# Kernel tuning notes

Measured on AMD Instinct MI355X. Metric: run time of the kernel, lower is better.

## Reference

```python
import jax, jax.numpy as jnp
import numpy as np

B, N = 1, 512
CS, CZ, H, CH, PQ, PV = 384, 128, 12, 16, 4, 8
INF, EPS = 1e5, 1e-8
SOFTPLUS_INV_1 = 0.541324854612918


def _init_linear(key, fan_in, fan_out):
    kw, kb = jax.random.split(key)
    std = float(1.0 / np.sqrt(fan_in))
    w = jax.random.normal(kw, (fan_in, fan_out), dtype=jnp.float32) * std
    b = jnp.zeros((fan_out,), dtype=jnp.float32)
    return w, b


def setup_inputs() -> dict:
    key = jax.random.key(0)
    ks = jax.random.split(key, 12)
    s = jax.random.normal(ks[0], (B, N, CS), dtype=jnp.float32)
    z = jax.random.normal(ks[1], (B, N, N, CZ), dtype=jnp.float32) * 0.1
    # proper rotation matrices via QR of random Gaussians
    rot, _ = jnp.linalg.qr(jax.random.normal(ks[2], (B, N, 3, 3), dtype=jnp.float32))
    trans = jax.random.normal(ks[3], (B, N, 3), dtype=jnp.float32) * 10.0
    mask = jnp.ones((B, N), dtype=jnp.float32)
    w_q, b_q = _init_linear(ks[4], CS, H * CH)
    w_kv, b_kv = _init_linear(ks[5], CS, 2 * H * CH)
    w_qp, b_qp = _init_linear(ks[6], CS, H * PQ * 3)
    w_kvp, b_kvp = _init_linear(ks[7], CS, H * (PQ + PV) * 3)
    w_b, b_b = _init_linear(ks[8], CZ, H)
    head_weights = jnp.full((H,), SOFTPLUS_INV_1, dtype=jnp.float32)
    concat_dim = H * (CZ + CH + PV * 4)
    # 'final' init -> zeros
    w_out = jnp.zeros((concat_dim, CS), dtype=jnp.float32)
    b_out = jnp.zeros((CS,), dtype=jnp.float32)
    return dict(s=s, z=z, rot=rot, trans=trans, mask=mask,
                w_q=w_q, b_q=b_q, w_kv=w_kv, b_kv=b_kv,
                w_qp=w_qp, b_qp=b_qp, w_kvp=w_kvp, b_kvp=b_kvp,
                w_b=w_b, b_b=b_b, head_weights=head_weights,
                w_out=w_out, b_out=b_out)


def reference(s, z, rot, trans, mask,
              w_q, b_q, w_kv, b_kv, w_qp, b_qp, w_kvp, b_kvp,
              w_b, b_b, head_weights, w_out, b_out):
    # scalar q/k/v: [B,N,H,CH]
    q = (s @ w_q + b_q).reshape(B, N, H, CH)
    kv = (s @ w_kv + b_kv).reshape(B, N, H, 2 * CH)
    k, v = kv[..., :CH], kv[..., CH:]

    def make_points(w, b, P):
        p = s @ w + b                                   # [B,N,3*H*P] (x|y|z chunks)
        p = jnp.moveaxis(p.reshape(B, N, 3, H * P), -2, -1)  # [B,N,H*P,3]
        p = jnp.einsum('bnij,bnpj->bnpi', rot, p) + trans[:, :, None]  # global frame
        return p.reshape(B, N, H, P, 3)

    q_pts = make_points(w_qp, b_qp, PQ)                 # [B,N,H,PQ,3]
    kv_pts = make_points(w_kvp, b_kvp, PQ + PV)
    k_pts, v_pts = kv_pts[..., :PQ, :], kv_pts[..., PQ:, :]

    # scalar QK attention + pair bias
    a = jnp.einsum('bqhc,bkhc->bhqk', q, k) * float(np.sqrt(1.0 / (3 * CH)))
    b_bias = z @ w_b + b_b                              # [B,N,N,H]
    a = a + float(np.sqrt(1.0 / 3.0)) * jnp.moveaxis(b_bias, -1, -3)

    # squared point-distance attention
    d = q_pts[:, :, None] - k_pts[:, None]              # [B,N,N,H,PQ,3]
    pt_att = jnp.sum(d * d, axis=-1)                    # [B,N,N,H,PQ]
    hw = jax.nn.softplus(head_weights) * float(np.sqrt(1.0 / (3 * (PQ * 9.0 / 2))))
    pt_att = -0.5 * jnp.sum(pt_att * hw[None, None, None, :, None], axis=-1)  # [B,N,N,H]
    a = a + jnp.moveaxis(pt_att, -1, -3)                # [B,H,N,N]

    sq_mask = (mask[:, :, None] * mask[:, None, :] - 1.0) * INF
    a = jax.nn.softmax(a + sq_mask[:, None], axis=-1)   # [B,H,N,N]

    # standard value path
    o = jnp.einsum('bhqk,bkhc->bqhc', a, v).reshape(B, N, H * CH)
    # point value path, rotated back to local frame
    o_pt = jnp.einsum('bhqk,bkhpc->bqhpc', a, v_pts)    # [B,N,H,PV,3]
    o_pt = jnp.einsum('bnji,bnhpj->bnhpi', rot, o_pt - trans[:, :, None, None])
    o_pt_norm = jnp.sqrt(jnp.sum(o_pt ** 2, axis=-1) + EPS).reshape(B, N, H * PV)
    o_pt = o_pt.reshape(B, N, H * PV, 3)
    # pair-weighted path
    o_pair = jnp.einsum('bhqk,bqkc->bqhc', a, z).reshape(B, N, H * CZ)

    o_cat = jnp.concatenate(
        [o, o_pt[..., 0], o_pt[..., 1], o_pt[..., 2], o_pt_norm, o_pair], axis=-1)
    return o_cat @ w_out + b_out
```

## Files before the change

kernel.cpp:

```cpp
#include <hip/hip_runtime.h>
#include <math.h>

#define NRES 512
#define CSD  384
#define CZD  128

#define OFF_Q     0
#define OFF_KT    98304
#define OFF_VC    196608
#define OFF_QP    458752
#define OFF_KPT   532480
#define OFF_A     606208
#define OFF_OCAT  3751936
#define OFF_WCAT  4833280
#define OFF_BCAT  (OFF_WCAT + 442368)
#define OFF_PRAWQ OFF_A
#define OFF_PRAWK (OFF_A + 73728)
#define OFF_PART  OFF_A

__global__ __launch_bounds__(256) void k_wcat(
    const float* __restrict__ w_q, const float* __restrict__ b_q,
    const float* __restrict__ w_kv, const float* __restrict__ b_kv,
    const float* __restrict__ w_qp, const float* __restrict__ b_qp,
    const float* __restrict__ w_kvp, const float* __restrict__ b_kvp,
    float* __restrict__ wcat, float* __restrict__ bcat)
{
    const int idx = blockIdx.x * 256 + threadIdx.x;
    if (idx < 442368) {
        const int k = idx / 1152, c = idx % 1152;
        float v;
        if (c < 192)      v = w_q[k*192 + c];
        else if (c < 576) v = w_kv[k*384 + (c - 192)];
        else if (c < 720) v = w_qp[k*144 + (c - 576)];
        else              v = w_kvp[k*432 + (c - 720)];
        wcat[idx] = v;
    } else if (idx < 443520) {
        const int c = idx - 442368;
        float v;
        if (c < 192)      v = b_q[c];
        else if (c < 576) v = b_kv[c - 192];
        else if (c < 720) v = b_qp[c - 576];
        else              v = b_kvp[c - 720];
        bcat[c] = v;
    }
}

__global__ __launch_bounds__(256) void k_proj2(
    const float* __restrict__ s, const float* __restrict__ wcat, const float* __restrict__ bcat,
    float* __restrict__ q, float* __restrict__ kkT, float* __restrict__ vcomb,
    float* __restrict__ praw_q, float* __restrict__ praw_kv)
{
    const int ct = blockIdx.x;
    const int n0 = blockIdx.y * 32;
    const int t = threadIdx.x;

    __shared__ float sT[32][34];
    __shared__ float wt[32][36];

    const int lr = t >> 3, lc4 = t & 7;
    const int tr = t >> 4, tc = t & 15;
    float4 sv4, wv4;

    sv4 = *(const float4*)&s[(n0 + lr) * CSD + lc4 * 4];
    wv4 = *(const float4*)&wcat[lr * 1152 + ct * 32 + lc4 * 4];
    sT[lc4*4+0][lr] = sv4.x; sT[lc4*4+1][lr] = sv4.y; sT[lc4*4+2][lr] = sv4.z; sT[lc4*4+3][lr] = sv4.w;
    *(float4*)&wt[lr][lc4*4] = wv4;
    __syncthreads();

    float a00 = 0.f, a01 = 0.f, a10 = 0.f, a11 = 0.f;

    for (int it = 0; it < 12; ++it) {
        if (it < 11) {
            const int k0 = (it + 1) * 32;
            sv4 = *(const float4*)&s[(n0 + lr) * CSD + k0 + lc4 * 4];
            wv4 = *(const float4*)&wcat[(k0 + lr) * 1152 + ct * 32 + lc4 * 4];
        }
        #pragma unroll
        for (int kx = 0; kx < 32; ++kx) {
            float2 ss = *(const float2*)&sT[kx][tr * 2];
            float2 ww = *(const float2*)&wt[kx][tc * 2];
            a00 += ss.x * ww.x; a01 += ss.x * ww.y;
            a10 += ss.y * ww.x; a11 += ss.y * ww.y;
        }
        __syncthreads();
        if (it < 11) {
            sT[lc4*4+0][lr] = sv4.x; sT[lc4*4+1][lr] = sv4.y; sT[lc4*4+2][lr] = sv4.z; sT[lc4*4+3][lr] = sv4.w;
            *(float4*)&wt[lr][lc4*4] = wv4;
            __syncthreads();
        }
    }

    float accv[2][2] = {{a00, a01}, {a10, a11}};
    #pragma unroll
    for (int i = 0; i < 2; ++i) {
        const int n = n0 + tr * 2 + i;
        #pragma unroll
        for (int j = 0; j < 2; ++j) {
            const int gcol = ct * 32 + tc * 2 + j;
            const float v = accv[i][j] + bcat[gcol];
            if (gcol < 192) {
                q[n*192 + gcol] = v;
            } else if (gcol < 576) {
                int g = gcol - 192, h = g >> 5, cc = g & 31;
                if (cc < 16) kkT[(h*16 + cc)*NRES + n] = v;
                else         vcomb[n*NRES + h*16 + (cc-16)] = v;
            } else if (gcol < 720) {
                praw_q[n*144 + (gcol - 576)] = v;
            } else {
                praw_kv[n*432 + (gcol - 720)] = v;
            }
        }
    }
}

__global__ __launch_bounds__(256) void k_rot(
    const float* __restrict__ praw_q, const float* __restrict__ praw_kv,
    const float* __restrict__ rot, const float* __restrict__ trans,
    float* __restrict__ q_pts, float* __restrict__ kptsT, float* __restrict__ vcomb)
{
    const int idx = blockIdx.x * 256 + threadIdx.x;
    const int n = idx / 192, u = idx % 192;
    const float* R = rot + n*9;
    const float* T = trans + n*3;
    float px, py, pz;
    if (u < 48) {
        px = praw_q[n*144 + u]; py = praw_q[n*144 + 48 + u]; pz = praw_q[n*144 + 96 + u];
    } else {
        int pt = u - 48;
        px = praw_kv[n*432 + pt]; py = praw_kv[n*432 + 144 + pt]; pz = praw_kv[n*432 + 288 + pt];
    }
    float x  = R[0]*px + R[1]*py + R[2]*pz + T[0];
    float y  = R[3]*px + R[4]*py + R[5]*pz + T[1];
    float zc = R[6]*px + R[7]*py + R[8]*pz + T[2];
    if (u < 48) {
        int o = (n*48 + u)*3;
        q_pts[o] = x; q_pts[o+1] = y; q_pts[o+2] = zc;
    } else {
        int pt = u - 48;
        int h = pt / 12, pp = pt % 12;
        if (pp < 4) {
            int dim = (h*4 + pp)*3;
            kptsT[(dim+0)*NRES + n] = x;
            kptsT[(dim+1)*NRES + n] = y;
            kptsT[(dim+2)*NRES + n] = zc;
        } else {
            int u2 = (h*8 + (pp-4))*3;
            vcomb[n*NRES + 192 + u2+0] = x;
            vcomb[n*NRES + 192 + u2+1] = y;
            vcomb[n*NRES + 192 + u2+2] = zc;
        }
    }
}

__global__ __launch_bounds__(256) void k_row(
    const float* __restrict__ z,
    const float* __restrict__ q, const float* __restrict__ kkT, const float* __restrict__ vcomb,
    const float* __restrict__ q_pts, const float* __restrict__ kptsT,
    const float* __restrict__ w_b, const float* __restrict__ b_b,
    const float* __restrict__ head_weights, const float* __restrict__ mask,
    const float* __restrict__ rot, const float* __restrict__ trans,
    float* __restrict__ o_cat)
{
    const int qn = blockIdx.x;
    const int t = threadIdx.x;

    __shared__ float zt[64*129];
    __shared__ float wb[128*12];
    __shared__ float part[4][64][13];
    __shared__ float a_lds[12][520];
    __shared__ float q_lds[192];
    __shared__ float qp_lds[144];
    __shared__ float hw_lds[12];
    __shared__ float optraw[288];

    for (int i = t; i < 1536; i += 256) wb[i] = w_b[i];
    if (t < 192) q_lds[t] = q[qn*192 + t];
    if (t < 144) qp_lds[t] = q_pts[qn*144 + t];
    if (t < 12)  hw_lds[t] = logf(1.f + expf(head_weights[t])) * 0.13608276f;

    const int kx = t & 63, qr = t >> 6;
    for (int kt = 0; kt < 8; ++kt) {
        const int k0 = kt*64;
        __syncthreads();
        const float4* zp4 = (const float4*)(z + ((size_t)qn*NRES + k0)*CZD);
        #pragma unroll
        for (int r = 0; r < 8; ++r) {
            int idx = t + r*256;
            int kk2 = idx >> 5, c4 = idx & 31;
            float4 v4 = zp4[idx];
            float* dst = &zt[kk2*129 + c4*4];
            dst[0]=v4.x; dst[1]=v4.y; dst[2]=v4.z; dst[3]=v4.w;
        }
        __syncthreads();
        float acc[12];
        #pragma unroll
        for (int h = 0; h < 12; ++h) acc[h] = 0.f;
        const float* zrow = &zt[kx*129 + qr*32];
        const float* wbp = &wb[qr*32*12];
        for (int c = 0; c < 32; ++c) {
            float zv = zrow[c];
            #pragma unroll
            for (int h = 0; h < 12; ++h) acc[h] += zv * wbp[c*12+h];
        }
        #pragma unroll
        for (int h = 0; h < 12; ++h) part[qr][kx][h] = acc[h];
        __syncthreads();
        for (int d = t; d < 768; d += 256) {
            int h = d >> 6, k2 = d & 63;
            a_lds[h][k0+k2] = b_b[h] + part[0][k2][h] + part[1][k2][h]
                            + part[2][k2][h] + part[3][k2][h];
        }
    }
    __syncthreads();

    const float mq = mask[qn];
    for (int h = 0; h < 12; ++h) {
        float qv[16], qpv[12];
        #pragma unroll
        for (int c = 0; c < 16; ++c) qv[c] = q_lds[h*16+c];
        #pragma unroll
        for (int d = 0; d < 12; ++d) qpv[d] = qp_lds[h*12+d];
        const float hw = hw_lds[h];
        const float* kT  = kkT + h*16*NRES;
        const float* kpT = kptsT + h*12*NRES;
        #pragma unroll
        for (int r = 0; r < 2; ++r) {
            const int kn = t + r*256;
            float acc = 0.f;
            #pragma unroll
            for (int c = 0; c < 16; ++c) acc += qv[c] * kT[c*NRES + kn];
            acc *= 0.14433757f;
            acc += 0.57735027f * a_lds[h][kn];
            float dsum = 0.f;
            #pragma unroll
            for (int d = 0; d < 12; ++d) { float df = qpv[d] - kpT[d*NRES + kn]; dsum += df*df; }
            a_lds[h][kn] = acc - 0.5f*hw*dsum + (mq*mask[kn]-1.f)*100000.f;
        }
    }
    __syncthreads();

    {
        const int w = t >> 6, lane = t & 63;
        for (int h = w; h < 12; h += 4) {
            float m = -1e30f;
            #pragma unroll
            for (int i = 0; i < 8; ++i) m = fmaxf(m, a_lds[h][lane + i*64]);
            #pragma unroll
            for (int off = 32; off > 0; off >>= 1) m = fmaxf(m, __shfl_xor(m, off));
            float ss = 0.f;
            #pragma unroll
            for (int i = 0; i < 8; ++i) {
                float e = __expf(a_lds[h][lane + i*64] - m);
                a_lds[h][lane + i*64] = e;
                ss += e;
            }
            #pragma unroll
            for (int off = 32; off > 0; off >>= 1) ss += __shfl_xor(ss, off);
            float inv = 1.f / ss;
            #pragma unroll
            for (int i = 0; i < 8; ++i) a_lds[h][lane + i*64] *= inv;
        }
    }
    __syncthreads();

    {
        const int c4 = t & 31, kgrp = t >> 5;
        const float4* zp = (const float4*)(z + (size_t)qn*NRES*CZD) + c4;
        float4 acc4[12];
        #pragma unroll
        for (int h = 0; h < 12; ++h) acc4[h] = make_float4(0.f,0.f,0.f,0.f);

        #pragma unroll 4
        for (int kn = kgrp; kn < NRES; kn += 8) {
            float4 zv = zp[kn*32];
            #pragma unroll
            for (int h = 0; h < 12; ++h) {
                float av = a_lds[h][kn];
                acc4[h].x += av*zv.x; acc4[h].y += av*zv.y;
                acc4[h].z += av*zv.z; acc4[h].w += av*zv.w;
            }
        }
        #pragma unroll
        for (int h = 0; h < 12; ++h) {
            acc4[h].x += __shfl_xor(acc4[h].x, 32);
            acc4[h].y += __shfl_xor(acc4[h].y, 32);
            acc4[h].z += __shfl_xor(acc4[h].z, 32);
            acc4[h].w += __shfl_xor(acc4[h].w, 32);
        }
        float (*ppart)[12][128] = (float (*)[12][128])zt;
        const int wave = t >> 6;
        if ((t & 63) < 32) {
            #pragma unroll
            for (int h = 0; h < 12; ++h) {
                ppart[wave][h][c4*4+0] = acc4[h].x;
                ppart[wave][h][c4*4+1] = acc4[h].y;
                ppart[wave][h][c4*4+2] = acc4[h].z;
                ppart[wave][h][c4*4+3] = acc4[h].w;
            }
        }
        __syncthreads();
        for (int i = t; i < 1536; i += 256) {
            int h = i >> 7, c = i & 127;
            float v = ppart[0][h][c] + ppart[1][h][c] + ppart[2][h][c] + ppart[3][h][c];
            o_cat[qn*2112 + 576 + h*128 + c] = v;
        }
    }

    {
        const int u0 = t;
        const int h0 = (u0 < 192) ? (u0 >> 4) : (u0 - 192) / 24;
        const int u1v = (t < 224) ? (t + 256) : 479;
        const int h1 = (u1v - 192) / 24;
        float acc0 = 0.f, acc1 = 0.f;
        const float* vp = vcomb;
        #pragma unroll 8
        for (int kn = 0; kn < NRES; ++kn) {
            const float* row = vp + (size_t)kn*NRES;
            acc0 += a_lds[h0][kn] * row[u0];
            acc1 += a_lds[h1][kn] * row[u1v];
        }
        if (u0 < 192) o_cat[qn*2112 + u0] = acc0;
        else          optraw[u0 - 192] = acc0;
        if (t < 224)  optraw[t + 64] = acc1;
    }
    __syncthreads();

    if (t < 96) {
        const float* R = rot + qn*9;
        const float* T = trans + qn*3;
        float ox = optraw[t*3]   - T[0];
        float oy = optraw[t*3+1] - T[1];
        float oz = optraw[t*3+2] - T[2];
        float x  = R[0]*ox + R[3]*oy + R[6]*oz;
        float y  = R[1]*ox + R[4]*oy + R[7]*oz;
        float zc = R[2]*ox + R[5]*oy + R[8]*oz;
        float* ob = o_cat + qn*2112;
        ob[192 + t] = x;
        ob[288 + t] = y;
        ob[384 + t] = zc;
        ob[480 + t] = sqrtf(x*x + y*y + zc*zc + 1e-8f);
    }
}

__global__ __launch_bounds__(256) void k_out2(
    const float* __restrict__ o_cat, const float* __restrict__ w_out, float* __restrict__ part)
{
    const int ct = blockIdx.x;
    const int n0 = blockIdx.y * 32;
    const int kc = blockIdx.z;
    const int t = threadIdx.x;

    __shared__ float oT[32][34];
    __shared__ float wt[32][36];

    const int lr = t >> 3, lc4 = t & 7;
    const int tr = t >> 4, tc = t & 15;
    const int kbase = kc * 352;
    float4 ov4, wv4;

    ov4 = *(const float4*)&o_cat[(n0 + lr) * 2112 + kbase + lc4 * 4];
    wv4 = *(const float4*)&w_out[(kbase + lr) * 384 + ct * 32 + lc4 * 4];
    oT[lc4*4+0][lr] = ov4.x; oT[lc4*4+1][lr] = ov4.y; oT[lc4*4+2][lr] = ov4.z; oT[lc4*4+3][lr] = ov4.w;
    *(float4*)&wt[lr][lc4*4] = wv4;
    __syncthreads();

    float a00 = 0.f, a01 = 0.f, a10 = 0.f, a11 = 0.f;

    for (int it = 0; it < 11; ++it) {
        if (it < 10) {
            const int k0 = kbase + (it + 1) * 32;
            ov4 = *(const float4*)&o_cat[(n0 + lr) * 2112 + k0 + lc4 * 4];
            wv4 = *(const float4*)&w_out[(k0 + lr) * 384 + ct * 32 + lc4 * 4];
        }
        #pragma unroll
        for (int kx = 0; kx < 32; ++kx) {
            float2 oo = *(const float2*)&oT[kx][tr * 2];
            float2 ww = *(const float2*)&wt[kx][tc * 2];
            a00 += oo.x * ww.x; a01 += oo.x * ww.y;
            a10 += oo.y * ww.x; a11 += oo.y * ww.y;
        }
        __syncthreads();
        if (it < 10) {
            oT[lc4*4+0][lr] = ov4.x; oT[lc4*4+1][lr] = ov4.y; oT[lc4*4+2][lr] = ov4.z; oT[lc4*4+3][lr] = ov4.w;
            *(float4*)&wt[lr][lc4*4] = wv4;
            __syncthreads();
        }
    }

    float* pp = part + (size_t)kc * 196608;
    pp[(n0 + tr*2 + 0)*384 + ct*32 + tc*2 + 0] = a00;
    pp[(n0 + tr*2 + 0)*384 + ct*32 + tc*2 + 1] = a01;
    pp[(n0 + tr*2 + 1)*384 + ct*32 + tc*2 + 0] = a10;
    pp[(n0 + tr*2 + 1)*384 + ct*32 + tc*2 + 1] = a11;
}

__global__ __launch_bounds__(256) void k_red(
    const float* __restrict__ part, const float* __restrict__ b_out, float* __restrict__ out)
{
    const int i = blockIdx.x*256 + threadIdx.x;
    float acc = b_out[i % 384];
    #pragma unroll
    for (int dc = 0; dc < 6; ++dc) acc += part[(size_t)dc*196608 + i];
    out[i] = acc;
}

extern "C" void kernel_launch(void* const* d_in, const int* in_sizes, int n_in,
                              void* d_out, int out_size, void* d_ws, size_t ws_size,
                              hipStream_t stream) {
    (void)in_sizes; (void)n_in; (void)out_size; (void)ws_size;
    const float* s      = (const float*)d_in[0];
    const float* z      = (const float*)d_in[1];
    const float* rot    = (const float*)d_in[2];
    const float* trans  = (const float*)d_in[3];
    const float* mask   = (const float*)d_in[4];
    const float* w_q    = (const float*)d_in[5];
    const float* b_q    = (const float*)d_in[6];
    const float* w_kv   = (const float*)d_in[7];
    const float* b_kv   = (const float*)d_in[8];
    const float* w_qp   = (const float*)d_in[9];
    const float* b_qp   = (const float*)d_in[10];
    const float* w_kvp  = (const float*)d_in[11];
    const float* b_kvp  = (const float*)d_in[12];
    const float* w_b    = (const float*)d_in[13];
    const float* b_b    = (const float*)d_in[14];
    const float* hwts   = (const float*)d_in[15];
    const float* w_out  = (const float*)d_in[16];
    const float* b_out  = (const float*)d_in[17];
    float* out = (float*)d_out;
    float* ws  = (float*)d_ws;

    float* q      = ws + OFF_Q;
    float* kkT    = ws + OFF_KT;
    float* vcomb  = ws + OFF_VC;
    float* qp     = ws + OFF_QP;
    float* kptsT  = ws + OFF_KPT;
    float* ocat   = ws + OFF_OCAT;
    float* wcat   = ws + OFF_WCAT;
    float* bcat   = ws + OFF_BCAT;
    float* part   = ws + OFF_PART;
    float* praw_q  = ws + OFF_PRAWQ;
    float* praw_kv = ws + OFF_PRAWK;

    k_wcat<<<dim3(1733), dim3(256), 0, stream>>>(w_q, b_q, w_kv, b_kv, w_qp, b_qp, w_kvp, b_kvp, wcat, bcat);
    k_proj2<<<dim3(36, 16), dim3(256), 0, stream>>>(s, wcat, bcat, q, kkT, vcomb, praw_q, praw_kv);
    k_rot<<<dim3(384), dim3(256), 0, stream>>>(praw_q, praw_kv, rot, trans, qp, kptsT, vcomb);
    k_row<<<dim3(NRES), dim3(256), 0, stream>>>(z, q, kkT, vcomb, qp, kptsT,
        w_b, b_b, hwts, mask, rot, trans, ocat);
    k_out2<<<dim3(12, 16, 6), dim3(256), 0, stream>>>(ocat, w_out, part);
    k_red<<<dim3(768), dim3(256), 0, stream>>>(part, b_out, out);
}
```

Before: 149.8 us.

## Fuse row attention into single-pass online softmax with register-prefetched z tiles

Rewrites the per-query row kernel to stream z in 64-key tiles once, computing pair bias, logits, an online softmax with running max and sum, and the z, scalar-value and point-value accumulations per tile. This removes the second full read of the z row from global memory and the full 12x512 logit buffer in shared memory. The next z tile is prefetched into registers while the current one is processed. In exchange it adds rescaling work and more barriers per tile, and raises register pressure from the 12 float4 accumulators plus 8 staging float4s.

```diff
diff --git a/kernel.cpp b/kernel.cpp
--- a/kernel.cpp
+++ b/kernel.cpp
@@ -152,7 +152,7 @@
     }
 }
 
-__global__ __launch_bounds__(256) void k_row(
+__global__ __launch_bounds__(256) void k_row2(
     const float* __restrict__ z,
     const float* __restrict__ q, const float* __restrict__ kkT, const float* __restrict__ vcomb,
     const float* __restrict__ q_pts, const float* __restrict__ kptsT,
@@ -164,10 +164,13 @@
     const int qn = blockIdx.x;
     const int t = threadIdx.x;
 
-    __shared__ float zt[64*129];
-    __shared__ float wb[128*12];
+    __shared__ float zt[64][132];
+    __shared__ float wb[1536];
     __shared__ float part[4][64][13];
-    __shared__ float a_lds[12][520];
+    __shared__ float bt[12][64];
+    __shared__ float pt[12][66];
+    __shared__ float fs[12];
+    __shared__ float ss[12];
     __shared__ float q_lds[192];
     __shared__ float qp_lds[144];
     __shared__ float hw_lds[12];
@@ -177,151 +180,188 @@
     if (t < 192) q_lds[t] = q[qn*192 + t];
     if (t < 144) qp_lds[t] = q_pts[qn*144 + t];
     if (t < 12)  hw_lds[t] = logf(1.f + expf(head_weights[t])) * 0.13608276f;
-
-    const int kx = t & 63, qr = t >> 6;
+    const float mq = mask[qn];
+
+    const int kx = t & 63, hgrp = t >> 6;
+    const int c4 = t & 31, kgrp = t >> 5;
+
+    float m_run0 = -1e30f, m_run1 = -1e30f, m_run2 = -1e30f;
+    float s_run0 = 0.f, s_run1 = 0.f, s_run2 = 0.f;
+    float4 opa[12];
+    #pragma unroll
+    for (int h = 0; h < 12; ++h) opa[h] = make_float4(0.f, 0.f, 0.f, 0.f);
+    float oacc0 = 0.f, oacc1 = 0.f;
+    const int u0 = t;
+    const int h0 = (u0 < 192) ? (u0 >> 4) : (u0 - 192) / 24;
+    const int u1 = t + 256;
+    const bool has_u1 = (u1 < 480);
+    const int h1 = has_u1 ? (u1 - 192) / 24 : 0;
+
+    float4 stg[8];
+    {
+        const float4* zp = (const float4*)(z + (size_t)qn * NRES * CZD);
+        #pragma unroll
+        for (int j = 0; j < 8; ++j) stg[j] = zp[t + j*256];
+        #pragma unroll
+        for (int j = 0; j < 8; ++j) {
+            int idx = t + j*256;
+            *(float4*)&zt[idx >> 5][(idx & 31) * 4] = stg[j];
+        }
+    }
+    __syncthreads();
+
     for (int kt = 0; kt < 8; ++kt) {
-        const int k0 = kt*64;
-        __syncthreads();
-        const float4* zp4 = (const float4*)(z + ((size_t)qn*NRES + k0)*CZD);
-        #pragma unroll
-        for (int r = 0; r < 8; ++r) {
-            int idx = t + r*256;
-            int kk2 = idx >> 5, c4 = idx & 31;
-            float4 v4 = zp4[idx];
-            float* dst = &zt[kk2*129 + c4*4];
-            dst[0]=v4.x; dst[1]=v4.y; dst[2]=v4.z; dst[3]=v4.w;
-        }
-        __syncthreads();
-        float acc[12];
-        #pragma unroll
-        for (int h = 0; h < 12; ++h) acc[h] = 0.f;
-        const float* zrow = &zt[kx*129 + qr*32];
-        const float* wbp = &wb[qr*32*12];
-        for (int c = 0; c < 32; ++c) {
-            float zv = zrow[c];
-            #pragma unroll
-            for (int h = 0; h < 12; ++h) acc[h] += zv * wbp[c*12+h];
-        }
-        #pragma unroll
-        for (int h = 0; h < 12; ++h) part[qr][kx][h] = acc[h];
+        const int k0 = kt * 64;
+
+        if (kt < 7) {
+            const float4* zp = (const float4*)(z + ((size_t)qn * NRES + k0 + 64) * CZD);
+            #pragma unroll
+            for (int j = 0; j < 8; ++j) stg[j] = zp[t + j*256];
+        }
+
+        {
+            float acc[12];
+            #pragma unroll
+            for (int h = 0; h < 12; ++h) acc[h] = 0.f;
+            #pragma unroll
+            for (int cc = 0; cc < 8; ++cc) {
+                float4 zv = *(const float4*)&zt[kx][hgrp*32 + cc*4];
+                const float* wp = &wb[(hgrp*32 + cc*4) * 12];
+                #pragma unroll
+                for (int h = 0; h < 12; ++h) acc[h] += zv.x * wp[h];
+                #pragma unroll
+                for (int h = 0; h < 12; ++h) acc[h] += zv.y * wp[12 + h];
+                #pragma unroll
+                for (int h = 0; h < 12; ++h) acc[h] += zv.z * wp[24 + h];
+                #pragma unroll
+                for (int h = 0; h < 12; ++h) acc[h] += zv.w * wp[36 + h];
+            }
+            #pragma unroll
+            for (int h = 0; h < 12; ++h) part[hgrp][kx][h] = acc[h];
+        }
         __syncthreads();
         for (int d = t; d < 768; d += 256) {
             int h = d >> 6, k2 = d & 63;
-            a_lds[h][k0+k2] = b_b[h] + part[0][k2][h] + part[1][k2][h]
-                            + part[2][k2][h] + part[3][k2][h];
-        }
+            bt[h][k2] = b_b[h] + part[0][k2][h] + part[1][k2][h] + part[2][k2][h] + part[3][k2][h];
+        }
+        __syncthreads();
+
+        {
+            const float mk = (mq * mask[k0 + kx] - 1.f) * 100000.f;
+            #pragma unroll
+            for (int hh = 0; hh < 3; ++hh) {
+                const int h = hgrp*3 + hh;
+                float acc = 0.f;
+                const float* kT = kkT + (h*16)*NRES + k0 + kx;
+                #pragma unroll
+                for (int c = 0; c < 16; ++c) acc += q_lds[h*16 + c] * kT[c*NRES];
+                acc *= 0.14433757f;
+                acc += 0.57735027f * bt[h][kx];
+                float dsum = 0.f;
+                const float* kpT = kptsT + (h*12)*NRES + k0 + kx;
+                #pragma unroll
+                for (int d = 0; d < 12; ++d) { float df = qp_lds[h*12 + d] - kpT[d*NRES]; dsum += df*df; }
+                float l = acc - 0.5f * hw_lds[h] * dsum + mk;
+
+                float m_old = (hh == 0) ? m_run0 : (hh == 1) ? m_run1 : m_run2;
+                float s_old = (hh == 0) ? s_run0 : (hh == 1) ? s_run1 : s_run2;
+                float pm = l;
+                #pragma unroll
+                for (int off = 32; off > 0; off >>= 1) pm = fmaxf(pm, __shfl_xor(pm, off));
+                float mnew = fmaxf(m_old, pm);
+                float f = __expf(m_old - mnew);
+                float p = __expf(l - mnew);
+                float psum = p;
+                #pragma unroll
+                for (int off = 32; off > 0; off >>= 1) psum += __shfl_xor(psum, off);
+                float snew = s_old * f + psum;
+                if (hh == 0) { m_run0 = mnew; s_run0 = snew; }
+                else if (hh == 1) { m_run1 = mnew; s_run1 = snew; }
+                else { m_run2 = mnew; s_run2 = snew; }
+                pt[h][kx] = p;
+                if (kx == 0) fs[h] = f;
+            }
+        }
+        __syncthreads();
+
+        {
+            #pragma unroll
+            for (int h = 0; h < 12; ++h) {
+                const float f = fs[h];
+                opa[h].x *= f; opa[h].y *= f; opa[h].z *= f; opa[h].w *= f;
+            }
+            #pragma unroll
+            for (int j = 0; j < 8; ++j) {
+                const int k = kgrp*8 + j;
+                float4 zv = *(const float4*)&zt[k][c4*4];
+                #pragma unroll
+                for (int h = 0; h < 12; ++h) {
+                    float pv = pt[h][k];
+                    opa[h].x += pv*zv.x; opa[h].y += pv*zv.y;
+                    opa[h].z += pv*zv.z; opa[h].w += pv*zv.w;
+                }
+            }
+            oacc0 *= fs[h0];
+            if (has_u1) oacc1 *= fs[h1];
+            const float* vb = vcomb + (size_t)k0 * NRES;
+            #pragma unroll 4
+            for (int k = 0; k < 64; ++k) {
+                const float* vrow = vb + (size_t)k * NRES;
+                oacc0 += pt[h0][k] * vrow[u0];
+                if (has_u1) oacc1 += pt[h1][k] * vrow[u1];
+            }
+        }
+        __syncthreads();
+
+        if (kt < 7) {
+            #pragma unroll
+            for (int j = 0; j < 8; ++j) {
+                int idx = t + j*256;
+                *(float4*)&zt[idx >> 5][(idx & 31) * 4] = stg[j];
+            }
+            __syncthreads();
+        }
+    }
+
+    if (kx == 0) {
+        ss[hgrp*3 + 0] = s_run0;
+        ss[hgrp*3 + 1] = s_run1;
+        ss[hgrp*3 + 2] = s_run2;
     }
     __syncthreads();
 
-    const float mq = mask[qn];
-    for (int h = 0; h < 12; ++h) {
-        float qv[16], qpv[12];
-        #pragma unroll
-        for (int c = 0; c < 16; ++c) qv[c] = q_lds[h*16+c];
-        #pragma unroll
-        for (int d = 0; d < 12; ++d) qpv[d] = qp_lds[h*12+d];
-        const float hw = hw_lds[h];
-        const float* kT  = kkT + h*16*NRES;
-        const float* kpT = kptsT + h*12*NRES;
-        #pragma unroll
-        for (int r = 0; r < 2; ++r) {
-            const int kn = t + r*256;
-            float acc = 0.f;
-            #pragma unroll
-            for (int c = 0; c < 16; ++c) acc += qv[c] * kT[c*NRES + kn];
-            acc *= 0.14433757f;
-            acc += 0.57735027f * a_lds[h][kn];
-            float dsum = 0.f;
-            #pragma unroll
-            for (int d = 0; d < 12; ++d) { float df = qpv[d] - kpT[d*NRES + kn]; dsum += df*df; }
-            a_lds[h][kn] = acc - 0.5f*hw*dsum + (mq*mask[kn]-1.f)*100000.f;
-        }
-    }
-    __syncthreads();
-
     {
-        const int w = t >> 6, lane = t & 63;
-        for (int h = w; h < 12; h += 4) {
-            float m = -1e30f;
-            #pragma unroll
-            for (int i = 0; i < 8; ++i) m = fmaxf(m, a_lds[h][lane + i*64]);
-            #pragma unroll
-            for (int off = 32; off > 0; off >>= 1) m = fmaxf(m, __shfl_xor(m, off));
-            float ss = 0.f;
-            #pragma unroll
-            for (int i = 0; i < 8; ++i) {
-                float e = __expf(a_lds[h][lane + i*64] - m);
-                a_lds[h][lane + i*64] = e;
-                ss += e;
-            }
-            #pragma unroll
-            for (int off = 32; off > 0; off >>= 1) ss += __shfl_xor(ss, off);
-            float inv = 1.f / ss;
-            #pragma unroll
-            for (int i = 0; i < 8; ++i) a_lds[h][lane + i*64] *= inv;
-        }
-    }
-    __syncthreads();
-
-    {
-        const int c4 = t & 31, kgrp = t >> 5;
-        const float4* zp = (const float4*)(z + (size_t)qn*NRES*CZD) + c4;
-        float4 acc4[12];
-        #pragma unroll
-        for (int h = 0; h < 12; ++h) acc4[h] = make_float4(0.f,0.f,0.f,0.f);
-
-        #pragma unroll 4
-        for (int kn = kgrp; kn < NRES; kn += 8) {
-            float4 zv = zp[kn*32];
-            #pragma unroll
-            for (int h = 0; h < 12; ++h) {
-                float av = a_lds[h][kn];
-                acc4[h].x += av*zv.x; acc4[h].y += av*zv.y;
-                acc4[h].z += av*zv.z; acc4[h].w += av*zv.w;
-            }
-        }
         #pragma unroll
         for (int h = 0; h < 12; ++h) {
-            acc4[h].x += __shfl_xor(acc4[h].x, 32);
-            acc4[h].y += __shfl_xor(acc4[h].y, 32);
-            acc4[h].z += __shfl_xor(acc4[h].z, 32);
-            acc4[h].w += __shfl_xor(acc4[h].w, 32);
-        }
-        float (*ppart)[12][128] = (float (*)[12][128])zt;
+            opa[h].x += __shfl_xor(opa[h].x, 32);
+            opa[h].y += __shfl_xor(opa[h].y, 32);
+            opa[h].z += __shfl_xor(opa[h].z, 32);
+            opa[h].w += __shfl_xor(opa[h].w, 32);
+        }
+        float (*pred)[12][128] = (float (*)[12][128])zt;
         const int wave = t >> 6;
         if ((t & 63) < 32) {
             #pragma unroll
             for (int h = 0; h < 12; ++h) {
-                ppart[wave][h][c4*4+0] = acc4[h].x;
-                ppart[wave][h][c4*4+1] = acc4[h].y;
-                ppart[wave][h][c4*4+2] = acc4[h].z;
-                ppart[wave][h][c4*4+3] = acc4[h].w;
+                pred[wave][h][c4*4+0] = opa[h].x;
+                pred[wave][h][c4*4+1] = opa[h].y;
+                pred[wave][h][c4*4+2] = opa[h].z;
+                pred[wave][h][c4*4+3] = opa[h].w;
             }
         }
         __syncthreads();
         for (int i = t; i < 1536; i += 256) {
             int h = i >> 7, c = i & 127;
-            float v = ppart[0][h][c] + ppart[1][h][c] + ppart[2][h][c] + ppart[3][h][c];
+            float v = (pred[0][h][c] + pred[1][h][c] + pred[2][h][c] + pred[3][h][c]) / ss[h];
             o_cat[qn*2112 + 576 + h*128 + c] = v;
         }
     }
 
     {
-        const int u0 = t;
-        const int h0 = (u0 < 192) ? (u0 >> 4) : (u0 - 192) / 24;
-        const int u1v = (t < 224) ? (t + 256) : 479;
-        const int h1 = (u1v - 192) / 24;
-        float acc0 = 0.f, acc1 = 0.f;
-        const float* vp = vcomb;
-        #pragma unroll 8
-        for (int kn = 0; kn < NRES; ++kn) {
-            const float* row = vp + (size_t)kn*NRES;
-            acc0 += a_lds[h0][kn] * row[u0];
-            acc1 += a_lds[h1][kn] * row[u1v];
-        }
-        if (u0 < 192) o_cat[qn*2112 + u0] = acc0;
-        else          optraw[u0 - 192] = acc0;
-        if (t < 224)  optraw[t + 64] = acc1;
+        float v0 = oacc0 / ss[h0];
+        if (u0 < 192) o_cat[qn*2112 + u0] = v0;
+        else          optraw[u0 - 192] = v0;
+        if (has_u1)   optraw[u1 - 192] = oacc1 / ss[h1];
     }
     __syncthreads();
 
@@ -444,7 +484,7 @@
     k_wcat<<<dim3(1733), dim3(256), 0, stream>>>(w_q, b_q, w_kv, b_kv, w_qp, b_qp, w_kvp, b_kvp, wcat, bcat);
     k_proj2<<<dim3(36, 16), dim3(256), 0, stream>>>(s, wcat, bcat, q, kkT, vcomb, praw_q, praw_kv);
     k_rot<<<dim3(384), dim3(256), 0, stream>>>(praw_q, praw_kv, rot, trans, qp, kptsT, vcomb);
-    k_row<<<dim3(NRES), dim3(256), 0, stream>>>(z, q, kkT, vcomb, qp, kptsT,
+    k_row2<<<dim3(NRES), dim3(256), 0, stream>>>(z, q, kkT, vcomb, qp, kptsT,
         w_b, b_b, hwts, mask, rot, trans, ocat);
     k_out2<<<dim3(12, 16, 6), dim3(256), 0, stream>>>(ocat, w_out, part);
     k_red<<<dim3(768), dim3(256), 0, stream>>>(part, b_out, out);
```

Result: slower. 464.8 us (+210.3%).

## Load z directly into registers for pair bias and shrink row kernel LDS

Applied to the files above, without the earlier changes.

The pair-bias projection in the per-row kernel now reads each z row straight from global memory into registers as float4s, with no staging through a padded LDS tile. This removes a large shared buffer and one barrier per tile, which lowers LDS use and may allow more blocks per CU. The value-path loop now reads float2 pairs with 240 threads instead of scalar reads with 256, and the z-weighted loop unroll goes from 4 to 8. The per-thread global reads of z are strided by row, so coalescing is worse than the old cooperative load, and the register use is higher.

```diff
diff --git a/kernel.cpp b/kernel.cpp
--- a/kernel.cpp
+++ b/kernel.cpp
@@ -152,7 +152,7 @@
     }
 }
 
-__global__ __launch_bounds__(256) void k_row(
+__global__ __launch_bounds__(256) void k_row3(
     const float* __restrict__ z,
     const float* __restrict__ q, const float* __restrict__ kkT, const float* __restrict__ vcomb,
     const float* __restrict__ q_pts, const float* __restrict__ kptsT,
@@ -164,54 +164,55 @@
     const int qn = blockIdx.x;
     const int t = threadIdx.x;
 
-    __shared__ float zt[64*129];
-    __shared__ float wb[128*12];
-    __shared__ float part[4][64][13];
-    __shared__ float a_lds[12][520];
+    __shared__ float U[6144];
+    __shared__ float a_lds[12][521];
     __shared__ float q_lds[192];
     __shared__ float qp_lds[144];
     __shared__ float hw_lds[12];
     __shared__ float optraw[288];
 
+    float* wb = U;
+    float (*part)[64][13] = (float (*)[64][13])&U[1536];
+
     for (int i = t; i < 1536; i += 256) wb[i] = w_b[i];
     if (t < 192) q_lds[t] = q[qn*192 + t];
     if (t < 144) qp_lds[t] = q_pts[qn*144 + t];
     if (t < 12)  hw_lds[t] = logf(1.f + expf(head_weights[t])) * 0.13608276f;
-
-    const int kx = t & 63, qr = t >> 6;
+    __syncthreads();
+
+    const int kx = t & 63, hgrp = t >> 6;
+
     for (int kt = 0; kt < 8; ++kt) {
         const int k0 = kt*64;
-        __syncthreads();
-        const float4* zp4 = (const float4*)(z + ((size_t)qn*NRES + k0)*CZD);
-        #pragma unroll
-        for (int r = 0; r < 8; ++r) {
-            int idx = t + r*256;
-            int kk2 = idx >> 5, c4 = idx & 31;
-            float4 v4 = zp4[idx];
-            float* dst = &zt[kk2*129 + c4*4];
-            dst[0]=v4.x; dst[1]=v4.y; dst[2]=v4.z; dst[3]=v4.w;
-        }
-        __syncthreads();
+        float4 zr[8];
+        const float4* zp = (const float4*)(z + ((size_t)qn*NRES + k0 + kx)*CZD + hgrp*32);
+        #pragma unroll
+        for (int j = 0; j < 8; ++j) zr[j] = zp[j];
         float acc[12];
         #pragma unroll
         for (int h = 0; h < 12; ++h) acc[h] = 0.f;
-        const float* zrow = &zt[kx*129 + qr*32];
-        const float* wbp = &wb[qr*32*12];
-        for (int c = 0; c < 32; ++c) {
-            float zv = zrow[c];
-            #pragma unroll
-            for (int h = 0; h < 12; ++h) acc[h] += zv * wbp[c*12+h];
-        }
-        #pragma unroll
-        for (int h = 0; h < 12; ++h) part[qr][kx][h] = acc[h];
+        #pragma unroll
+        for (int j = 0; j < 8; ++j) {
+            const float* wp = &wb[(hgrp*32 + j*4) * 12];
+            #pragma unroll
+            for (int h = 0; h < 12; ++h) acc[h] += zr[j].x * wp[h];
+            #pragma unroll
+            for (int h = 0; h < 12; ++h) acc[h] += zr[j].y * wp[12 + h];
+            #pragma unroll
+            for (int h = 0; h < 12; ++h) acc[h] += zr[j].z * wp[24 + h];
+            #pragma unroll
+            for (int h = 0; h < 12; ++h) acc[h] += zr[j].w * wp[36 + h];
+        }
+        #pragma unroll
+        for (int h = 0; h < 12; ++h) part[hgrp][kx][h] = acc[h];
         __syncthreads();
         for (int d = t; d < 768; d += 256) {
             int h = d >> 6, k2 = d & 63;
-            a_lds[h][k0+k2] = b_b[h] + part[0][k2][h] + part[1][k2][h]
-                            + part[2][k2][h] + part[3][k2][h];
-        }
-    }
-    __syncthreads();
+            a_lds[h][k0 + k2] = b_b[h] + part[0][k2][h] + part[1][k2][h]
+                              + part[2][k2][h] + part[3][k2][h];
+        }
+        __syncthreads();
+    }
 
     const float mq = mask[qn];
     for (int h = 0; h < 12; ++h) {
@@ -270,7 +271,7 @@
         #pragma unroll
         for (int h = 0; h < 12; ++h) acc4[h] = make_float4(0.f,0.f,0.f,0.f);
 
-        #pragma unroll 4
+        #pragma unroll 8
         for (int kn = kgrp; kn < NRES; kn += 8) {
             float4 zv = zp[kn*32];
             #pragma unroll
@@ -287,41 +288,41 @@
             acc4[h].z += __shfl_xor(acc4[h].z, 32);
             acc4[h].w += __shfl_xor(acc4[h].w, 32);
         }
-        float (*ppart)[12][128] = (float (*)[12][128])zt;
+        float (*pred)[12][128] = (float (*)[12][128])U;
         const int wave = t >> 6;
         if ((t & 63) < 32) {
             #pragma unroll
             for (int h = 0; h < 12; ++h) {
-                ppart[wave][h][c4*4+0] = acc4[h].x;
-                ppart[wave][h][c4*4+1] = acc4[h].y;
-                ppart[wave][h][c4*4+2] = acc4[h].z;
-                ppart[wave][h][c4*4+3] = acc4[h].w;
+                pred[wave][h][c4*4+0] = acc4[h].x;
+                pred[wave][h][c4*4+1] = acc4[h].y;
+                pred[wave][h][c4*4+2] = acc4[h].z;
+                pred[wave][h][c4*4+3] = acc4[h].w;
             }
         }
         __syncthreads();
         for (int i = t; i < 1536; i += 256) {
             int h = i >> 7, c = i & 127;
-            float v = ppart[0][h][c] + ppart[1][h][c] + ppart[2][h][c] + ppart[3][h][c];
+            float v = pred[0][h][c] + pred[1][h][c] + pred[2][h][c] + pred[3][h][c];
             o_cat[qn*2112 + 576 + h*128 + c] = v;
         }
     }
 
-    {
-        const int u0 = t;
-        const int h0 = (u0 < 192) ? (u0 >> 4) : (u0 - 192) / 24;
-        const int u1v = (t < 224) ? (t + 256) : 479;
-        const int h1 = (u1v - 192) / 24;
-        float acc0 = 0.f, acc1 = 0.f;
-        const float* vp = vcomb;
+    if (t < 240) {
+        const int ch0 = 2*t, ch1 = 2*t + 1;
+        const int hA = (ch0 < 192) ? (ch0 >> 4) : (ch0 - 192) / 24;
+        const int hB = (ch1 < 192) ? (ch1 >> 4) : (ch1 - 192) / 24;
+        float aAcc = 0.f, bAcc = 0.f;
+        const float2* vp2 = (const float2*)vcomb + t;
         #pragma unroll 8
         for (int kn = 0; kn < NRES; ++kn) {
-            const float* row = vp + (size_t)kn*NRES;
-            acc0 += a_lds[h0][kn] * row[u0];
-            acc1 += a_lds[h1][kn] * row[u1v];
-        }
-        if (u0 < 192) o_cat[qn*2112 + u0] = acc0;
-        else          optraw[u0 - 192] = acc0;
-        if (t < 224)  optraw[t + 64] = acc1;
+            float2 v = vp2[(size_t)kn*256];
+            aAcc += a_lds[hA][kn] * v.x;
+            bAcc += a_lds[hB][kn] * v.y;
+        }
+        if (ch0 < 192) o_cat[qn*2112 + ch0] = aAcc;
+        else           optraw[ch0 - 192] = aAcc;
+        if (ch1 < 192) o_cat[qn*2112 + ch1] = bAcc;
+        else           optraw[ch1 - 192] = bAcc;
     }
     __syncthreads();
 
@@ -444,7 +445,7 @@
     k_wcat<<<dim3(1733), dim3(256), 0, stream>>>(w_q, b_q, w_kv, b_kv, w_qp, b_qp, w_kvp, b_kvp, wcat, bcat);
     k_proj2<<<dim3(36, 16), dim3(256), 0, stream>>>(s, wcat, bcat, q, kkT, vcomb, praw_q, praw_kv);
     k_rot<<<dim3(384), dim3(256), 0, stream>>>(praw_q, praw_kv, rot, trans, qp, kptsT, vcomb);
-    k_row<<<dim3(NRES), dim3(256), 0, stream>>>(z, q, kkT, vcomb, qp, kptsT,
+    k_row3<<<dim3(NRES), dim3(256), 0, stream>>>(z, q, kkT, vcomb, qp, kptsT,
         w_b, b_b, hwts, mask, rot, trans, ocat);
     k_out2<<<dim3(12, 16, 6), dim3(256), 0, stream>>>(ocat, w_out, part);
     k_red<<<dim3(768), dim3(256), 0, stream>>>(part, b_out, out);
```

Result: slower. 235.3 us (+57.1%).
